# Kernel tuning notes

Measured on AMD Instinct MI355X. Metric: run time of the kernel, lower is better.

## Reference

```python
import jax, jax.numpy as jnp
import numpy as np

B, L, D, H = 2, 2048, 2048, 16
DH = D // H

def setup_inputs() -> dict:
    key = jax.random.key(0)
    ks = jax.random.split(key, 7)
    q = jax.random.normal(ks[0], (B, L, D), dtype=jnp.float32)
    k = jax.random.normal(ks[1], (B, L, D), dtype=jnp.float32)
    v = jax.random.normal(ks[2], (B, L, D), dtype=jnp.float32)
    # causal mask: True means masked (matches torch masked_fill semantics)
    attn_mask = jnp.triu(jnp.ones((L, L), dtype=bool), k=1)[None, None, :, :]
    scale = 0.02
    wq = jax.random.normal(ks[3], (D, D), dtype=jnp.float32) * scale
    wk = jax.random.normal(ks[4], (D, D), dtype=jnp.float32) * scale
    wv = jax.random.normal(ks[5], (D, D), dtype=jnp.float32) * scale
    wo = jax.random.normal(ks[6], (D, D), dtype=jnp.float32) * scale
    return {"q": q, "k": k, "v": v, "attn_mask": attn_mask,
            "wq": wq, "wk": wk, "wv": wv, "wo": wo}

def _split_heads(x):
    b, l, _ = x.shape
    return x.reshape(b, l, H, DH).transpose(0, 2, 1, 3)  # [B,H,L,DH]

def reference(q, k, v, attn_mask, wq, wk, wv, wo):
    # torch Linear: y = x @ W.T (bias=False)
    qh = _split_heads(q @ wq.T)
    kh = _split_heads(k @ wk.T)
    vh = _split_heads(v @ wv.T)
    scale = 1.0 / np.sqrt(DH).astype(np.float32)
    scores = jnp.einsum('bhqd,bhkd->bhqk', qh, kh) * scale
    neg = jnp.finfo(scores.dtype).min
    scores = jnp.where(attn_mask, neg, scores)
    attn = jax.nn.softmax(scores, axis=-1)
    ctx = jnp.einsum('bhqk,bhkd->bhqd', attn, vh)
    ctx = ctx.transpose(0, 2, 1, 3).reshape(q.shape[0], q.shape[1], D)
    return ctx @ wo.T
```

## Files before the change

kernel.cpp:

```cpp
#include <hip/hip_runtime.h>

#define B_  2
#define L_  2048
#define D_  2048
#define H_  16
#define DH_ 128
#define K_  2048

typedef __attribute__((ext_vector_type(8))) short bf16x8;
typedef __attribute__((ext_vector_type(4))) float f32x4;
typedef __attribute__((ext_vector_type(4))) float float4v;
typedef __attribute__((ext_vector_type(8))) unsigned short u16x8;
typedef __attribute__((ext_vector_type(4))) unsigned short u16x4;

__device__ __forceinline__ unsigned short f2bf(float f) {
  unsigned u = __builtin_bit_cast(unsigned, f);
  u += 0x7fffu + ((u >> 16) & 1u);
  return (unsigned short)(u >> 16);
}

typedef __attribute__((address_space(3))) unsigned int lds_uint;
typedef __attribute__((address_space(1))) const unsigned int glob_uint;
__device__ __forceinline__ void gld16(const void* g, void* l) {
  __builtin_amdgcn_global_load_lds((glob_uint*)g, (lds_uint*)l, 16, 0, 0);
}

#define BAR() do { asm volatile("" ::: "memory"); __builtin_amdgcn_s_barrier(); asm volatile("" ::: "memory"); } while (0)
#define VMCNT(n) asm volatile("s_waitcnt vmcnt(" #n ")" ::: "memory")

__global__ void cvt_all(const float* __restrict__ wq, const float* __restrict__ wk,
                        const float* __restrict__ wv, const float* __restrict__ wo,
                        const float* __restrict__ q, const float* __restrict__ k,
                        const float* __restrict__ v, unsigned short* __restrict__ ws,
                        int nacts) {
  const size_t DD = (size_t)D_ * D_;
  const size_t BLD = (size_t)B_ * L_ * D_;
  const int z = blockIdx.z;
  const float* src;
  unsigned short* dst;
  size_t nelem;
  if (z < 4) {
    src = (z == 0) ? wq : (z == 1) ? wk : (z == 2) ? wv : wo;
    dst = ws + (size_t)z * DD;
    nelem = DD;
  } else {
    if (z - 4 >= nacts) return;
    src = (z == 4) ? q : (z == 5) ? k : v;
    dst = ws + 4 * DD + (size_t)(z - 4) * BLD;
    nelem = BLD;
  }
  size_t i = ((size_t)blockIdx.x * 256 + threadIdx.x) * 8;
  if (i >= nelem) return;
  float4v x0 = *(const float4v*)(src + i);
  float4v x1 = *(const float4v*)(src + i + 4);
  u16x8 p;
  p[0]=f2bf(x0[0]); p[1]=f2bf(x0[1]); p[2]=f2bf(x0[2]); p[3]=f2bf(x0[3]);
  p[4]=f2bf(x1[0]); p[5]=f2bf(x1[1]); p[6]=f2bf(x1[2]); p[7]=f2bf(x1[3]);
  *(u16x8*)(dst + i) = p;
}

__global__ __launch_bounds__(512, 2) void gemm256(
    const unsigned short* __restrict__ a0, const unsigned short* __restrict__ a1,
    const unsigned short* __restrict__ a2,
    const unsigned short* __restrict__ w0, const unsigned short* __restrict__ w1,
    const unsigned short* __restrict__ w2,
    unsigned short* __restrict__ Qh, unsigned short* __restrict__ Kh,
    unsigned short* __restrict__ Vt) {
  __shared__ unsigned short smem[2 * 32768];

  const int lin = blockIdx.x + 16 * (blockIdx.y + 8 * blockIdx.z);
  const int s = (lin & 7) * 48 + (lin >> 3);
  const int mt = s & 15;
  const int r_ = s >> 4;
  const int ntile = r_ & 7;
  const int z = r_ >> 3;

  const unsigned short* A = (z == 0) ? a0 : (z == 1) ? a1 : a2;
  const unsigned short* W = (z == 0) ? w0 : (z == 1) ? w1 : w2;

  const int bm0 = mt * 256;
  const int bn0 = ntile * 256;

  const int tid = threadIdx.x;
  const int wid = tid >> 6, lane = tid & 63;
  const int wr = wid >> 2;
  const int wc = wid & 3;
  const int l15 = lane & 15, l4 = lane >> 4;

  const unsigned short* gsrc[8];
  int ldst[8];
#pragma unroll
  for (int i = 0; i < 4; ++i) {
    const int c = i * 512 + tid, r = c >> 3, s0 = c & 7;
    gsrc[i] = A + (size_t)(bm0 + r) * K_ + ((s0 ^ (r & 7)) << 3);
    ldst[i] = c * 8;
    gsrc[4 + i] = W + (size_t)(bn0 + r) * K_ + ((s0 ^ (r & 7)) << 3);
    ldst[4 + i] = 16384 + c * 8;
  }
#define STAGE(idx, p) do { gld16(gsrc[idx], &smem[(p) * 32768 + ldst[idx]]); gsrc[idx] += 64; } while (0)

  int offA[8][2], offB[4][2];
#pragma unroll
  for (int mf = 0; mf < 8; ++mf)
#pragma unroll
    for (int ks = 0; ks < 2; ++ks) {
      const int row = wr * 128 + mf * 16 + l15;
      const int ch = ks * 4 + l4;
      offA[mf][ks] = row * 64 + ((ch ^ (row & 7)) << 3);
    }
#pragma unroll
  for (int nf = 0; nf < 4; ++nf)
#pragma unroll
    for (int ks = 0; ks < 2; ++ks) {
      const int rowb = wc * 64 + nf * 16 + l15;
      const int ch = ks * 4 + l4;
      offB[nf][ks] = 16384 + rowb * 64 + ((ch ^ (rowb & 7)) << 3);
    }

  f32x4 acc[8][4];
#pragma unroll
  for (int m = 0; m < 8; ++m)
#pragma unroll
    for (int n = 0; n < 4; ++n) { f32x4 zz = {0.f, 0.f, 0.f, 0.f}; acc[m][n] = zz; }

  STAGE(0, 0); STAGE(1, 0); STAGE(2, 0); STAGE(3, 0);
  STAGE(4, 0); STAGE(5, 0); STAGE(6, 0); STAGE(7, 0);
  VMCNT(0);
  BAR();

  int p = 0;
  for (int t = 0; t < 32; ++t) {
    const int p2 = p ^ 1;
    if (t < 31) {
      STAGE(0, p2); STAGE(1, p2); STAGE(2, p2); STAGE(3, p2);
      STAGE(4, p2); STAGE(5, p2); STAGE(6, p2); STAGE(7, p2);
    }
    const unsigned short* bA = &smem[p * 32768];
    bf16x8 bfr[4][2];
#pragma unroll
    for (int nf = 0; nf < 4; ++nf)
#pragma unroll
      for (int ks = 0; ks < 2; ++ks)
        bfr[nf][ks] = *(const bf16x8*)&bA[offB[nf][ks]];
    __builtin_amdgcn_s_setprio(1);
#pragma unroll
    for (int mf = 0; mf < 8; ++mf) {
      bf16x8 a0f = *(const bf16x8*)&bA[offA[mf][0]];
      bf16x8 a1f = *(const bf16x8*)&bA[offA[mf][1]];
#pragma unroll
      for (int nf = 0; nf < 4; ++nf) {
        acc[mf][nf] = __builtin_amdgcn_mfma_f32_16x16x32_bf16(a0f, bfr[nf][0], acc[mf][nf], 0, 0, 0);
        acc[mf][nf] = __builtin_amdgcn_mfma_f32_16x16x32_bf16(a1f, bfr[nf][1], acc[mf][nf], 0, 0, 0);
      }
    }
    __builtin_amdgcn_s_setprio(0);
    VMCNT(0);
    BAR();
    p = p2;
  }
#undef STAGE

  if (z < 2) {
    unsigned short* O = (z == 0) ? Qh : Kh;
#pragma unroll
    for (int mf = 0; mf < 8; ++mf) {
      const int rr = bm0 + wr * 128 + mf * 16 + l4 * 4;
#pragma unroll
      for (int nf = 0; nf < 4; ++nf) {
        const int cc = bn0 + wc * 64 + nf * 16 + l15;
        const int h = cc >> 7, dh = cc & 127;
#pragma unroll
        for (int j = 0; j < 4; ++j) {
          const int r2 = rr + j;
          O[((size_t)((r2 >> 11) * H_ + h) * L_ + (r2 & 2047)) * DH_ + dh] = f2bf(acc[mf][nf][j]);
        }
      }
    }
  } else {
    unsigned short* T = smem;
    const int b = bm0 >> 11, lb = bm0 & 2047;
#pragma unroll 1
    for (int half = 0; half < 2; ++half) {
      if (half) __syncthreads();
      if (wr == half) {
#pragma unroll
        for (int mf = 0; mf < 8; ++mf) {
          const int rl = mf * 16 + l4 * 4;
#pragma unroll
          for (int nf = 0; nf < 4; ++nf) {
            const int cl = wc * 64 + nf * 16 + l15;
            u16x4 vv;
#pragma unroll
            for (int j = 0; j < 4; ++j) vv[j] = f2bf(acc[mf][nf][j]);
            *(u16x4*)&T[cl * 144 + rl] = vv;
          }
        }
      }
      __syncthreads();
#pragma unroll
      for (int it = 0; it < 8; ++it) {
        const int idx = it * 512 + tid;
        const int rT = idx >> 4, cT = idx & 15;
        u16x8 val = *(const u16x8*)&T[rT * 144 + cT * 8];
        const int n = bn0 + rT, h = n >> 7, dh = n & 127;
        *(u16x8*)&Vt[((size_t)(b * H_ + h) * DH_ + dh) * L_ + lb + half * 128 + cT * 8] = val;
      }
    }
  }
}

__global__ __launch_bounds__(512, 2) void gemm8o(
    const unsigned short* __restrict__ A, const unsigned short* __restrict__ W,
    float* __restrict__ OF) {
  __shared__ unsigned short smem[3 * 24576];

  const int lin = blockIdx.x + 32 * blockIdx.y;
  const int s = (lin & 7) * 32 + (lin >> 3);
  const int mt = s & 31;
  const int ntile = s >> 5;

  const int bm0 = mt * 128;
  const int bn0 = ntile * 256;

  const int tid = threadIdx.x;
  const int wid = tid >> 6, lane = tid & 63;
  const int wr = wid >> 2, wc = wid & 3;
  const int l15 = lane & 15, l4 = lane >> 4;

  const unsigned short* gsrc[6];
  int ldst[6];
  {
#pragma unroll
    for (int i = 0; i < 2; ++i) {
      const int c = i * 512 + tid, r = c >> 3, s0 = c & 7;
      gsrc[i] = A + (size_t)(bm0 + r) * K_ + ((s0 ^ (r & 7)) << 3);
      ldst[i] = c * 8;
    }
#pragma unroll
    for (int u = 0; u < 2; ++u)
#pragma unroll
      for (int i = 0; i < 2; ++i) {
        const int c = i * 512 + tid, r = c >> 3, s0 = c & 7;
        gsrc[2 + u * 2 + i] = W + (size_t)(bn0 + u * 128 + r) * K_ + ((s0 ^ (r & 7)) << 3);
        ldst[2 + u * 2 + i] = 8192 + (u * 1024 + c) * 8;
      }
  }
#define STAGE(idx, p) do { gld16(gsrc[idx], &smem[(p) * 24576 + ldst[idx]]); gsrc[idx] += 64; } while (0)

  int offA[4][2], offB[4][2];
#pragma unroll
  for (int mf = 0; mf < 4; ++mf)
#pragma unroll
    for (int ks = 0; ks < 2; ++ks) {
      const int row = wr * 64 + mf * 16 + l15;
      const int ch = ks * 4 + l4;
      offA[mf][ks] = row * 64 + ((ch ^ (row & 7)) << 3);
    }
#pragma unroll
  for (int nf = 0; nf < 4; ++nf)
#pragma unroll
    for (int ks = 0; ks < 2; ++ks) {
      const int rowb = wc * 64 + nf * 16 + l15;
      const int ch = ks * 4 + l4;
      offB[nf][ks] = 8192 + rowb * 64 + ((ch ^ (rowb & 7)) << 3);
    }

  f32x4 acc[4][4];
#pragma unroll
  for (int m = 0; m < 4; ++m)
#pragma unroll
    for (int n = 0; n < 4; ++n) { f32x4 zz = {0.f, 0.f, 0.f, 0.f}; acc[m][n] = zz; }

  STAGE(0, 0); STAGE(1, 0); STAGE(2, 0); STAGE(3, 0); STAGE(4, 0); STAGE(5, 0);
  STAGE(0, 1); STAGE(1, 1); STAGE(2, 1); STAGE(3, 1); STAGE(4, 1); STAGE(5, 1);
  VMCNT(6);
  BAR();

  int p = 0;
  for (int t = 0; t < 32; ++t) {
    int p2 = p + 2; if (p2 >= 3) p2 -= 3;
    const unsigned short* bA = &smem[p * 24576];
    bf16x8 af[4][2], bfr[4][2];
#pragma unroll
    for (int mf = 0; mf < 4; ++mf)
#pragma unroll
      for (int ks = 0; ks < 2; ++ks)
        af[mf][ks] = *(const bf16x8*)&bA[offA[mf][ks]];
#pragma unroll
    for (int nf = 0; nf < 4; ++nf)
#pragma unroll
      for (int ks = 0; ks < 2; ++ks)
        bfr[nf][ks] = *(const bf16x8*)&bA[offB[nf][ks]];
    if (t < 30) { STAGE(0, p2); STAGE(1, p2); STAGE(2, p2); STAGE(3, p2); STAGE(4, p2); STAGE(5, p2); }
    __builtin_amdgcn_s_setprio(1);
#pragma unroll
    for (int mf = 0; mf < 4; ++mf)
#pragma unroll
      for (int nf = 0; nf < 4; ++nf)
#pragma unroll
        for (int ks = 0; ks < 2; ++ks)
          acc[mf][nf] = __builtin_amdgcn_mfma_f32_16x16x32_bf16(af[mf][ks], bfr[nf][ks], acc[mf][nf], 0, 0, 0);
    __builtin_amdgcn_s_setprio(0);
    if (t < 30) { VMCNT(6); } else { VMCNT(0); }
    BAR();
    p = (p == 2) ? 0 : p + 1;
  }
#undef STAGE

#pragma unroll
  for (int mf = 0; mf < 4; ++mf) {
    const int rr = bm0 + wr * 64 + mf * 16 + l4 * 4;
#pragma unroll
    for (int nf = 0; nf < 4; ++nf) {
      const int cc = bn0 + wc * 64 + nf * 16 + l15;
#pragma unroll
      for (int j = 0; j < 4; ++j) OF[(size_t)(rr + j) * D_ + cc] = acc[mf][nf][j];
    }
  }
}

__global__ __launch_bounds__(256, 2) void proj_gemm_f32a(
    const float* __restrict__ q, const float* __restrict__ k, const float* __restrict__ v,
    const unsigned short* __restrict__ wqb, const unsigned short* __restrict__ wkb,
    const unsigned short* __restrict__ wvb,
    unsigned short* __restrict__ Qh, unsigned short* __restrict__ Kh,
    unsigned short* __restrict__ Vt) {
  __shared__ unsigned short smem[128 * 136];
  unsigned short* As = smem;
  unsigned short* Bs = smem + 128 * 64;

  const int z = blockIdx.z;
  const float* A = (z == 0) ? q : (z == 1) ? k : v;
  const unsigned short* W = (z == 0) ? wqb : (z == 1) ? wkb : wvb;

  const int tid = threadIdx.x;
  const int wave = tid >> 6, lane = tid & 63;
  const int wr = wave >> 1, wc = wave & 1;
  const int bm0 = blockIdx.x * 128;
  const int bn0 = blockIdx.y * 128;
  const int l15 = lane & 15, l4 = lane >> 4;

  f32x4 acc[4][4];
#pragma unroll
  for (int m = 0; m < 4; m++)
#pragma unroll
    for (int n = 0; n < 4; n++) { f32x4 zz = {0.f, 0.f, 0.f, 0.f}; acc[m][n] = zz; }

  for (int k0 = 0; k0 < K_; k0 += 64) {
#pragma unroll
    for (int it = 0; it < 4; ++it) {
      const int base = it * 256 + wave * 64;
      const int ch = base + lane;
      const int r = ch >> 3, c = ch & 7;
      gld16(W + (size_t)(bn0 + r) * K_ + (k0 + c * 8), Bs + base * 8);
    }
#pragma unroll
    for (int it = 0; it < 4; ++it) {
      const int ch = it * 256 + tid;
      const int r = ch >> 3, c = ch & 7;
      const float* g = A + (size_t)(bm0 + r) * K_ + (k0 + c * 8);
      float4v x0 = *(const float4v*)g;
      float4v x1 = *(const float4v*)(g + 4);
      u16x8 pp;
      pp[0]=f2bf(x0[0]); pp[1]=f2bf(x0[1]); pp[2]=f2bf(x0[2]); pp[3]=f2bf(x0[3]);
      pp[4]=f2bf(x1[0]); pp[5]=f2bf(x1[1]); pp[6]=f2bf(x1[2]); pp[7]=f2bf(x1[3]);
      *(u16x8*)&As[ch * 8] = pp;
    }
    __syncthreads();
#pragma unroll
    for (int ks = 0; ks < 2; ++ks) {
      const int kc = ks * 32 + l4 * 8;
      bf16x8 af[4], bfr[4];
#pragma unroll
      for (int m = 0; m < 4; m++) af[m] = *(const bf16x8*)&As[(wr * 64 + m * 16 + l15) * 64 + kc];
#pragma unroll
      for (int n = 0; n < 4; n++) bfr[n] = *(const bf16x8*)&Bs[(wc * 64 + n * 16 + l15) * 64 + kc];
#pragma unroll
      for (int m = 0; m < 4; m++)
#pragma unroll
        for (int n = 0; n < 4; n++)
          acc[m][n] = __builtin_amdgcn_mfma_f32_16x16x32_bf16(af[m], bfr[n], acc[m][n], 0, 0, 0);
    }
    __syncthreads();
  }

  if (z < 2) {
    unsigned short* O = (z == 0) ? Qh : Kh;
#pragma unroll
    for (int m = 0; m < 4; m++) {
      const int rr = bm0 + wr * 64 + m * 16 + l4 * 4;
#pragma unroll
      for (int n = 0; n < 4; n++) {
        const int cc = bn0 + wc * 64 + n * 16 + l15;
        const int h = cc >> 7, dh = cc & 127;
#pragma unroll
        for (int j = 0; j < 4; j++) {
          const int r2 = rr + j;
          O[((size_t)((r2 >> 11) * H_ + h) * L_ + (r2 & 2047)) * DH_ + dh] = f2bf(acc[m][n][j]);
        }
      }
    }
  } else {
    __syncthreads();
    unsigned short* T = smem;
#pragma unroll
    for (int m = 0; m < 4; m++)
#pragma unroll
      for (int n = 0; n < 4; n++) {
        const int cl = wc * 64 + n * 16 + l15;
        const int rl = wr * 64 + m * 16 + l4 * 4;
#pragma unroll
        for (int j = 0; j < 4; j++) T[cl * 136 + rl + j] = f2bf(acc[m][n][j]);
      }
    __syncthreads();
    const int b = bm0 >> 11, lbase = bm0 & 2047;
    const int hb = bn0 >> 7;
#pragma unroll
    for (int it = 0; it < 8; ++it) {
      const int idx = it * 256 + tid;
      const int dhl = idx >> 4, c = idx & 15;
      u16x8 val = *(const u16x8*)&T[dhl * 136 + c * 8];
      *(u16x8*)&Vt[((size_t)(b * H_ + hb) * DH_ + dhl) * L_ + lbase + c * 8] = val;
    }
  }
}

#define SCALE_ 0.08838834764831845f

__global__ __launch_bounds__(512, 2) void attn_kernel(
    const unsigned short* __restrict__ Qh, const unsigned short* __restrict__ Kh,
    const unsigned short* __restrict__ Vt, unsigned short* __restrict__ ctx) {
  __shared__ unsigned short Ks[128 * 128];
  __shared__ unsigned short Vs[128 * 128];
  __shared__ unsigned short Ps[8][16 * 128];

  const int pair = blockIdx.x, bh = blockIdx.y;
  const size_t hoff = (size_t)bh * L_ * DH_;
  const unsigned short* Qp = Qh + hoff;
  const unsigned short* Kp = Kh + hoff;
  const unsigned short* Vp = Vt + hoff;

  const int tid = threadIdx.x, wave = tid >> 6, lane = tid & 63;
  const int l15 = lane & 15, l4 = lane >> 4;
  const int b = bh >> 4, h = bh & 15;

#pragma unroll 1
  for (int p = 0; p < 2; ++p) {
    const int qt = p ? (15 - pair) : pair;
    const int ntiles = qt + 1;

    bf16x8 qf[4];
    {
      const int qrow = qt * 128 + wave * 16 + l15;
#pragma unroll
      for (int s = 0; s < 4; s++)
        qf[s] = *(const bf16x8*)&Qp[(size_t)qrow * DH_ + s * 32 + l4 * 8];
    }

    f32x4 o[8];
#pragma unroll
    for (int df = 0; df < 8; df++) { f32x4 zz = {0.f, 0.f, 0.f, 0.f}; o[df] = zz; }
    float m_r[4] = {-1e30f, -1e30f, -1e30f, -1e30f};
    float l_r[4] = {0.f, 0.f, 0.f, 0.f};

    for (int kt = 0; kt < ntiles; ++kt) {
#pragma unroll
      for (int it = 0; it < 4; ++it) {
        const int ch = it * 512 + tid;
        const int r = ch >> 4, s = ch & 15;
        gld16(Kp + (size_t)(kt * 128 + r) * DH_ + ((s ^ (r & 7)) * 8), (unsigned short*)Ks + ch * 8);
      }
#pragma unroll
      for (int it = 0; it < 4; ++it) {
        const int ch = it * 512 + tid;
        const int r = ch >> 4, s = ch & 15;
        gld16(Vp + (size_t)r * L_ + kt * 128 + ((s ^ (r & 7)) * 8), (unsigned short*)Vs + ch * 8);
      }
      __syncthreads();

      f32x4 sa[8];
#pragma unroll
      for (int f = 0; f < 8; f++) { f32x4 zz = {0.f, 0.f, 0.f, 0.f}; sa[f] = zz; }
      __builtin_amdgcn_s_setprio(1);
#pragma unroll
      for (int ks = 0; ks < 4; ++ks) {
        const int c = ks * 4 + l4;
#pragma unroll
        for (int f = 0; f < 8; ++f) {
          const int n = f * 16 + l15;
          bf16x8 kf = *(const bf16x8*)&Ks[n * 128 + ((c ^ (n & 7)) * 8)];
          sa[f] = __builtin_amdgcn_mfma_f32_16x16x32_bf16(qf[ks], kf, sa[f], 0, 0, 0);
        }
      }
      __builtin_amdgcn_s_setprio(0);

      const bool last = (kt == qt);
#pragma unroll
      for (int f = 0; f < 8; f++) {
        const int kg = kt * 128 + f * 16 + l15;
#pragma unroll
        for (int j = 0; j < 4; j++) {
          float t = sa[f][j] * SCALE_;
          if (last && kg > qt * 128 + wave * 16 + l4 * 4 + j) t = -1e30f;
          sa[f][j] = t;
        }
      }

#pragma unroll
      for (int j = 0; j < 4; j++) {
        float mx = fmaxf(fmaxf(fmaxf(sa[0][j], sa[1][j]), fmaxf(sa[2][j], sa[3][j])),
                         fmaxf(fmaxf(sa[4][j], sa[5][j]), fmaxf(sa[6][j], sa[7][j])));
#pragma unroll
        for (int d = 1; d < 16; d <<= 1) mx = fmaxf(mx, __shfl_xor(mx, d));
        const float mnew = fmaxf(m_r[j], mx);
        const float alpha = __expf(m_r[j] - mnew);
        float rs = 0.f;
        const int row = l4 * 4 + j;
#pragma unroll
        for (int f = 0; f < 8; f++) {
          float pp = __expf(sa[f][j] - mnew);
          rs += pp;
          const int col = f * 16 + l15;
          const int c = col >> 3;
          Ps[wave][row * 128 + ((c ^ (row & 7)) * 8) + (col & 7)] = f2bf(pp);
        }
#pragma unroll
        for (int d = 1; d < 16; d <<= 1) rs += __shfl_xor(rs, d);
        l_r[j] = l_r[j] * alpha + rs;
        m_r[j] = mnew;
#pragma unroll
        for (int df = 0; df < 8; df++) o[df][j] *= alpha;
      }

      __builtin_amdgcn_s_setprio(1);
#pragma unroll
      for (int ksl = 0; ksl < 4; ++ksl) {
        const int pc = ksl * 4 + l4;
        bf16x8 pf = *(const bf16x8*)&Ps[wave][l15 * 128 + ((pc ^ (l15 & 7)) * 8)];
#pragma unroll
        for (int df = 0; df < 8; ++df) {
          const int vr = df * 16 + l15;
          bf16x8 vf = *(const bf16x8*)&Vs[vr * 128 + ((pc ^ (vr & 7)) * 8)];
          o[df] = __builtin_amdgcn_mfma_f32_16x16x32_bf16(pf, vf, o[df], 0, 0, 0);
        }
      }
      __builtin_amdgcn_s_setprio(0);
      __syncthreads();
    }

#pragma unroll
    for (int j = 0; j < 4; j++) {
      const float inv = 1.0f / l_r[j];
      const int lq = qt * 128 + wave * 16 + l4 * 4 + j;
      const size_t rowb = ((size_t)(b * L_ + lq)) * D_ + h * DH_;
#pragma unroll
      for (int df = 0; df < 8; ++df)
        ctx[rowb + df * 16 + l15] = f2bf(o[df][j] * inv);
    }
  }
}

extern "C" void kernel_launch(void* const* d_in, const int* in_sizes, int n_in,
                              void* d_out, int out_size, void* d_ws, size_t ws_size,
                              hipStream_t stream) {
  const float* q  = (const float*)d_in[0];
  const float* k  = (const float*)d_in[1];
  const float* v  = (const float*)d_in[2];
  const float* wq = (const float*)d_in[4];
  const float* wk = (const float*)d_in[5];
  const float* wv = (const float*)d_in[6];
  const float* wo = (const float*)d_in[7];

  const size_t DD = (size_t)D_ * D_;
  const size_t BLD = (size_t)B_ * L_ * D_;
  unsigned short* ws  = (unsigned short*)d_ws;
  unsigned short* wqb = ws;
  unsigned short* wkb = wqb + DD;
  unsigned short* wvb = wkb + DD;
  unsigned short* wob = wvb + DD;

  const size_t need_full = (4 * DD + 7 * BLD) * 2;

  if (ws_size >= need_full) {
    unsigned short* qb  = wob + DD;
    unsigned short* kb  = qb + BLD;
    unsigned short* vb  = kb + BLD;
    unsigned short* QhP = vb + BLD;
    unsigned short* KhP = QhP + BLD;
    unsigned short* VtP = KhP + BLD;
    unsigned short* ctx = VtP + BLD;

    cvt_all<<<dim3(4096, 1, 7), 256, 0, stream>>>(wq, wk, wv, wo, q, k, v, ws, 3);
    gemm256<<<dim3(16, 8, 3), 512, 0, stream>>>(qb, kb, vb, wqb, wkb, wvb, QhP, KhP, VtP);
    attn_kernel<<<dim3(8, 32), 512, 0, stream>>>(QhP, KhP, VtP, ctx);
    gemm8o<<<dim3(32, 8), 512, 0, stream>>>(ctx, wob, (float*)d_out);
  } else {
    unsigned short* QhP = wob + DD;
    unsigned short* KhP = QhP + BLD;
    unsigned short* VtP = KhP + BLD;
    unsigned short* ctx = VtP + BLD;

    cvt_all<<<dim3(4096, 1, 4), 256, 0, stream>>>(wq, wk, wv, wo, q, k, v, ws, 0);
    proj_gemm_f32a<<<dim3(32, 16, 3), 256, 0, stream>>>(q, k, v, wqb, wkb, wvb, QhP, KhP, VtP);
    attn_kernel<<<dim3(8, 32), 512, 0, stream>>>(QhP, KhP, VtP, ctx);
    gemm8o<<<dim3(32, 8), 512, 0, stream>>>(ctx, wob, (float*)d_out);
  }
}
```

Before: 289.7 us.

## Double-buffer K tiles in attention, remap blocks, split Q projection GEMM

The attention kernel now double-buffers K tiles in LDS: the next K tile is prefetched while the current scores are computed, and V loads overlap the softmax. It also remaps block indices so that the 8 q-tile pairs of each head are spread across the grid. The Q projection moves out of the 3-way 256x256 GEMM into a separate launch of the 128x256 output-GEMM kernel, now templated for a bf16 head-split epilogue. This balances wave counts across CUs and hides global load latency, at the cost of an extra kernel launch and more LDS in attention.

```diff
diff --git a/kernel.cpp b/kernel.cpp
--- a/kernel.cpp
+++ b/kernel.cpp
@@ -61,22 +61,19 @@
 
 __global__ __launch_bounds__(512, 2) void gemm256(
     const unsigned short* __restrict__ a0, const unsigned short* __restrict__ a1,
-    const unsigned short* __restrict__ a2,
     const unsigned short* __restrict__ w0, const unsigned short* __restrict__ w1,
-    const unsigned short* __restrict__ w2,
-    unsigned short* __restrict__ Qh, unsigned short* __restrict__ Kh,
-    unsigned short* __restrict__ Vt) {
+    unsigned short* __restrict__ Kh, unsigned short* __restrict__ Vt) {
   __shared__ unsigned short smem[2 * 32768];
 
   const int lin = blockIdx.x + 16 * (blockIdx.y + 8 * blockIdx.z);
-  const int s = (lin & 7) * 48 + (lin >> 3);
+  const int s = (lin & 7) * 32 + (lin >> 3);
   const int mt = s & 15;
   const int r_ = s >> 4;
   const int ntile = r_ & 7;
   const int z = r_ >> 3;
 
-  const unsigned short* A = (z == 0) ? a0 : (z == 1) ? a1 : a2;
-  const unsigned short* W = (z == 0) ? w0 : (z == 1) ? w1 : w2;
+  const unsigned short* A = z ? a1 : a0;
+  const unsigned short* W = z ? w1 : w0;
 
   const int bm0 = mt * 256;
   const int bn0 = ntile * 256;
@@ -160,8 +157,7 @@
   }
 #undef STAGE
 
-  if (z < 2) {
-    unsigned short* O = (z == 0) ? Qh : Kh;
+  if (z == 0) {
 #pragma unroll
     for (int mf = 0; mf < 8; ++mf) {
       const int rr = bm0 + wr * 128 + mf * 16 + l4 * 4;
@@ -172,7 +168,7 @@
 #pragma unroll
         for (int j = 0; j < 4; ++j) {
           const int r2 = rr + j;
-          O[((size_t)((r2 >> 11) * H_ + h) * L_ + (r2 & 2047)) * DH_ + dh] = f2bf(acc[mf][nf][j]);
+          Kh[((size_t)((r2 >> 11) * H_ + h) * L_ + (r2 & 2047)) * DH_ + dh] = f2bf(acc[mf][nf][j]);
         }
       }
     }
@@ -209,9 +205,10 @@
   }
 }
 
-__global__ __launch_bounds__(512, 2) void gemm8o(
+template <int OUT>
+__global__ __launch_bounds__(512, 2) void gemm8p(
     const unsigned short* __restrict__ A, const unsigned short* __restrict__ W,
-    float* __restrict__ OF) {
+    void* __restrict__ outp) {
   __shared__ unsigned short smem[3 * 24576];
 
   const int lin = blockIdx.x + 32 * blockIdx.y;
@@ -307,14 +304,33 @@
   }
 #undef STAGE
 
-#pragma unroll
-  for (int mf = 0; mf < 4; ++mf) {
-    const int rr = bm0 + wr * 64 + mf * 16 + l4 * 4;
-#pragma unroll
-    for (int nf = 0; nf < 4; ++nf) {
-      const int cc = bn0 + wc * 64 + nf * 16 + l15;
-#pragma unroll
-      for (int j = 0; j < 4; ++j) OF[(size_t)(rr + j) * D_ + cc] = acc[mf][nf][j];
+  if (OUT == 0) {
+    float* OF = (float*)outp;
+#pragma unroll
+    for (int mf = 0; mf < 4; ++mf) {
+      const int rr = bm0 + wr * 64 + mf * 16 + l4 * 4;
+#pragma unroll
+      for (int nf = 0; nf < 4; ++nf) {
+        const int cc = bn0 + wc * 64 + nf * 16 + l15;
+#pragma unroll
+        for (int j = 0; j < 4; ++j) OF[(size_t)(rr + j) * D_ + cc] = acc[mf][nf][j];
+      }
+    }
+  } else {
+    unsigned short* O = (unsigned short*)outp;
+#pragma unroll
+    for (int mf = 0; mf < 4; ++mf) {
+      const int rr = bm0 + wr * 64 + mf * 16 + l4 * 4;
+#pragma unroll
+      for (int nf = 0; nf < 4; ++nf) {
+        const int cc = bn0 + wc * 64 + nf * 16 + l15;
+        const int h = cc >> 7, dh = cc & 127;
+#pragma unroll
+        for (int j = 0; j < 4; ++j) {
+          const int r2 = rr + j;
+          O[((size_t)((r2 >> 11) * H_ + h) * L_ + (r2 & 2047)) * DH_ + dh] = f2bf(acc[mf][nf][j]);
+        }
+      }
     }
   }
 }
@@ -430,11 +446,14 @@
 __global__ __launch_bounds__(512, 2) void attn_kernel(
     const unsigned short* __restrict__ Qh, const unsigned short* __restrict__ Kh,
     const unsigned short* __restrict__ Vt, unsigned short* __restrict__ ctx) {
-  __shared__ unsigned short Ks[128 * 128];
+  __shared__ unsigned short Ks[2][128 * 128];
   __shared__ unsigned short Vs[128 * 128];
   __shared__ unsigned short Ps[8][16 * 128];
 
-  const int pair = blockIdx.x, bh = blockIdx.y;
+  const int lin0 = blockIdx.x + 8 * blockIdx.y;
+  const int w = (lin0 & 7) * 32 + (lin0 >> 3);
+  const int pair = w & 7, bh = w >> 3;
+
   const size_t hoff = (size_t)bh * L_ * DH_;
   const unsigned short* Qp = Qh + hoff;
   const unsigned short* Kp = Kh + hoff;
@@ -444,10 +463,25 @@
   const int l15 = lane & 15, l4 = lane >> 4;
   const int b = bh >> 4, h = bh & 15;
 
+#define STAGEK(kt, buf) do { \
+  _Pragma("unroll") \
+  for (int it = 0; it < 4; ++it) { \
+    const int ch = it * 512 + tid; \
+    const int r = ch >> 4, s2 = ch & 15; \
+    gld16(Kp + (size_t)((kt) * 128 + r) * DH_ + ((s2 ^ (r & 7)) * 8), (unsigned short*)&Ks[buf][0] + ch * 8); \
+  } } while (0)
+#define STAGEV(kt) do { \
+  _Pragma("unroll") \
+  for (int it = 0; it < 4; ++it) { \
+    const int ch = it * 512 + tid; \
+    const int r = ch >> 4, s2 = ch & 15; \
+    gld16(Vp + (size_t)r * L_ + (kt) * 128 + ((s2 ^ (r & 7)) * 8), (unsigned short*)Vs + ch * 8); \
+  } } while (0)
+
 #pragma unroll 1
-  for (int p = 0; p < 2; ++p) {
-    const int qt = p ? (15 - pair) : pair;
-    const int ntiles = qt + 1;
+  for (int pp = 0; pp < 2; ++pp) {
+    const int qt = pp ? (15 - pair) : pair;
+    const int nt = qt + 1;
 
     bf16x8 qf[4];
     {
@@ -463,20 +497,15 @@
     float m_r[4] = {-1e30f, -1e30f, -1e30f, -1e30f};
     float l_r[4] = {0.f, 0.f, 0.f, 0.f};
 
-    for (int kt = 0; kt < ntiles; ++kt) {
-#pragma unroll
-      for (int it = 0; it < 4; ++it) {
-        const int ch = it * 512 + tid;
-        const int r = ch >> 4, s = ch & 15;
-        gld16(Kp + (size_t)(kt * 128 + r) * DH_ + ((s ^ (r & 7)) * 8), (unsigned short*)Ks + ch * 8);
-      }
-#pragma unroll
-      for (int it = 0; it < 4; ++it) {
-        const int ch = it * 512 + tid;
-        const int r = ch >> 4, s = ch & 15;
-        gld16(Vp + (size_t)r * L_ + kt * 128 + ((s ^ (r & 7)) * 8), (unsigned short*)Vs + ch * 8);
-      }
-      __syncthreads();
+    int p = 0;
+    STAGEK(0, 0);
+    VMCNT(0);
+    BAR();
+
+#pragma unroll 1
+    for (int kt = 0; kt < nt; ++kt) {
+      if (kt + 1 < nt) STAGEK(kt + 1, p ^ 1);
+      STAGEV(kt);
 
       f32x4 sa[8];
 #pragma unroll
@@ -488,7 +517,7 @@
 #pragma unroll
         for (int f = 0; f < 8; ++f) {
           const int n = f * 16 + l15;
-          bf16x8 kf = *(const bf16x8*)&Ks[n * 128 + ((c ^ (n & 7)) * 8)];
+          bf16x8 kf = *(const bf16x8*)&Ks[p][n * 128 + ((c ^ (n & 7)) * 8)];
           sa[f] = __builtin_amdgcn_mfma_f32_16x16x32_bf16(qf[ks], kf, sa[f], 0, 0, 0);
         }
       }
@@ -518,11 +547,11 @@
         const int row = l4 * 4 + j;
 #pragma unroll
         for (int f = 0; f < 8; f++) {
-          float pp = __expf(sa[f][j] - mnew);
-          rs += pp;
+          float pv = __expf(sa[f][j] - mnew);
+          rs += pv;
           const int col = f * 16 + l15;
           const int c = col >> 3;
-          Ps[wave][row * 128 + ((c ^ (row & 7)) * 8) + (col & 7)] = f2bf(pp);
+          Ps[wave][row * 128 + ((c ^ (row & 7)) * 8) + (col & 7)] = f2bf(pv);
         }
 #pragma unroll
         for (int d = 1; d < 16; d <<= 1) rs += __shfl_xor(rs, d);
@@ -531,6 +560,9 @@
 #pragma unroll
         for (int df = 0; df < 8; df++) o[df][j] *= alpha;
       }
+
+      VMCNT(0);
+      BAR();
 
       __builtin_amdgcn_s_setprio(1);
 #pragma unroll
@@ -545,7 +577,8 @@
         }
       }
       __builtin_amdgcn_s_setprio(0);
-      __syncthreads();
+      BAR();
+      p ^= 1;
     }
 
 #pragma unroll
@@ -558,6 +591,8 @@
         ctx[rowb + df * 16 + l15] = f2bf(o[df][j] * inv);
     }
   }
+#undef STAGEK
+#undef STAGEV
 }
 
 extern "C" void kernel_launch(void* const* d_in, const int* in_sizes, int n_in,
@@ -591,9 +626,10 @@
     unsigned short* ctx = VtP + BLD;
 
     cvt_all<<<dim3(4096, 1, 7), 256, 0, stream>>>(wq, wk, wv, wo, q, k, v, ws, 3);
-    gemm256<<<dim3(16, 8, 3), 512, 0, stream>>>(qb, kb, vb, wqb, wkb, wvb, QhP, KhP, VtP);
+    gemm256<<<dim3(16, 8, 2), 512, 0, stream>>>(kb, vb, wkb, wvb, KhP, VtP);
+    gemm8p<1><<<dim3(32, 8), 512, 0, stream>>>(qb, wqb, QhP);
     attn_kernel<<<dim3(8, 32), 512, 0, stream>>>(QhP, KhP, VtP, ctx);
-    gemm8o<<<dim3(32, 8), 512, 0, stream>>>(ctx, wob, (float*)d_out);
+    gemm8p<0><<<dim3(32, 8), 512, 0, stream>>>(ctx, wob, d_out);
   } else {
     unsigned short* QhP = wob + DD;
     unsigned short* KhP = QhP + BLD;
@@ -603,6 +639,6 @@
     cvt_all<<<dim3(4096, 1, 4), 256, 0, stream>>>(wq, wk, wv, wo, q, k, v, ws, 0);
     proj_gemm_f32a<<<dim3(32, 16, 3), 256, 0, stream>>>(q, k, v, wqb, wkb, wvb, QhP, KhP, VtP);
     attn_kernel<<<dim3(8, 32), 512, 0, stream>>>(QhP, KhP, VtP, ctx);
-    gemm8o<<<dim3(32, 8), 512, 0, stream>>>(ctx, wob, (float*)d_out);
-  }
-}
+    gemm8p<0><<<dim3(32, 8), 512, 0, stream>>>(ctx, wob, d_out);
+  }
+}
```

New measurement: 265.6 us. 8.3% less time.
